# Optimization experiments

Hardware: AMD Instinct MI355X
Metric: run time of the kernel (lower is better)

Reference implementation:

```python
import jax, jax.numpy as jnp
from jax import lax
import numpy as np

STATE, ACT, TGT = 115, 39, 3
DIMS = [STATE + ACT, 16, 32, 64, 128, 64, 32, 16, 8, STATE]
B, T = 2048, 128


def setup_inputs() -> dict:
    key = jax.random.key(0)
    ks = jax.random.split(key, 2 * 9 + 3)
    inp = {"u": jax.random.normal(ks[0], (B, T, STATE + ACT), jnp.float32)}
    for i in range(9):
        fi, fo = DIMS[i], DIMS[i + 1]
        s = 1.0 / np.sqrt(fi)
        inp[f"W{i}"] = jax.random.uniform(ks[2 * i + 1], (fi, fo), jnp.float32, -s, s)
        inp[f"b{i}"] = jax.random.uniform(ks[2 * i + 2], (fo,), jnp.float32, -s, s)
    s = 1.0 / np.sqrt(STATE)
    inp["Wr"] = jax.random.uniform(ks[-2], (STATE, TGT), jnp.float32, -s, s)
    inp["br"] = jax.random.uniform(ks[-1], (TGT,), jnp.float32, -s, s)
    return inp


def reference(u, W0, b0, W1, b1, W2, b2, W3, b3, W4, b4, W5, b5, W6, b6, W7, b7, W8, b8, Wr, br):
    Ws = [W0, W1, W2, W3, W4, W5, W6, W7, W8]
    bs = [b0, b1, b2, b3, b4, b5, b6, b7, b8]

    def mlp(h):
        # 8 hidden Linear+ReLU6 layers, final Linear with no activation
        for i in range(8):
            h = jnp.clip(h @ Ws[i] + bs[i], 0.0, 6.0)  # ReLU6
        return h @ Ws[8] + bs[8]

    x0 = u[:, 0, :STATE]                      # [B, S]
    acts = jnp.swapaxes(u[:, :, -ACT:], 0, 1)  # [T, B, A]

    def step(x, a):
        xn = x + mlp(jnp.concatenate([x, a], axis=1))  # residual update
        return xn, xn

    _, xs = lax.scan(step, x0, acts)          # xs: [T, B, S] = x[:,1:,:]
    x_full = jnp.concatenate([x0[None], xs], axis=0)      # [T+1, B, S]
    x_full = jnp.swapaxes(x_full, 0, 1)                   # [B, T+1, S]

    r = x_full[:, 1:, :] @ Wr + br                        # [B, T, TGT]
    reward = -jnp.sqrt(jnp.sum(r * r, axis=2, keepdims=True))  # [B, T, 1]
    return jnp.concatenate([x_full[:, :-1, :], reward], axis=2)  # [B, T, S+1]
```

## Files before the change

### kernel.cpp

```cpp
#include <hip/hip_runtime.h>
#include <math.h>


#define TSTEPS 128
#define NB     2048
#define NST    115
#define NACT   39
#define NINF   154
#define NOUTF  116
constexpr int NT   = 256;
constexpr int ROWS = 4;

template<int CTRL>
__device__ __forceinline__ float dpp_add(float x) {
  int y = __builtin_amdgcn_update_dpp(0, __float_as_int(x), CTRL, 0xF, 0xF, true);
  return x + __int_as_float(y);
}
template<int KS>
__device__ __forceinline__ float kreduce(float a) {
  if constexpr (KS >= 2)  a = dpp_add<0xB1>(a);
  if constexpr (KS >= 4)  a = dpp_add<0x4E>(a);
  if constexpr (KS >= 8)  a = dpp_add<0x141>(a);
  if constexpr (KS >= 16) a = dpp_add<0x140>(a);
  return a;
}

__device__ __forceinline__ void barrier_lds() {
  asm volatile("s_waitcnt lgkmcnt(0)\n\ts_barrier" ::: "memory");
}
__device__ __forceinline__ void wait_lds() {
  asm volatile("s_waitcnt lgkmcnt(0)" ::: "memory");
}

template<int K, int NW, int NP, int NC, int KS, int RS, int J>
__device__ __forceinline__ void wload(const float* __restrict__ Wg,
                                      const float* __restrict__ bg,
                                      float (&w)[J][NC], float (&b)[NC], int tid) {
  static_assert(NP * KS * RS == NT, "bad cfg");
  constexpr float BS = 1.0f / (float)KS;
  const int kp = tid % KS, rest = tid / KS, cg = rest % NP;
#pragma unroll
  for (int j = 0; j < J; ++j)
#pragma unroll
    for (int c = 0; c < NC; ++c) {
      const int k = kp + KS * j, n = cg + c * NP;
      w[j][c] = (k < K && n < NW) ? Wg[k * NW + n] : 0.f;
    }
#pragma unroll
  for (int c = 0; c < NC; ++c) {
    const int n = cg + c * NP;
    b[c] = (n < NW) ? bg[n] * BS : 0.f;
  }
}

template<int K, int NW, int NP, int NC, int KS, int RS, int J, bool CLIP>
__device__ __forceinline__ void lrun(const float (&w)[J][NC], const float (&b)[NC],
                                     const float* __restrict__ in,
                                     float* __restrict__ out, int tid) {
  constexpr int RPL = ROWS / RS;
  const int kp = tid % KS, rest = tid / KS, cg = rest % NP, rg = rest / NP;
  float acc[NC][RPL];
#pragma unroll
  for (int c = 0; c < NC; ++c)
#pragma unroll
    for (int r = 0; r < RPL; ++r) acc[c][r] = b[c];

#pragma unroll
  for (int j = 0; j < J; ++j) {
    const int k = kp + KS * j;
    const float* ap = in + k * ROWS + rg * RPL;
    float av[RPL];
    if constexpr (RPL == 4) {
      float4 t = *(const float4*)ap; av[0]=t.x; av[1]=t.y; av[2]=t.z; av[3]=t.w;
    } else if constexpr (RPL == 2) {
      float2 t = *(const float2*)ap; av[0]=t.x; av[1]=t.y;
    } else {
      av[0] = *ap;
    }
#pragma unroll
    for (int c = 0; c < NC; ++c)
#pragma unroll
      for (int r = 0; r < RPL; ++r) acc[c][r] += w[j][c] * av[r];
  }
#pragma unroll
  for (int c = 0; c < NC; ++c)
#pragma unroll
    for (int r = 0; r < RPL; ++r) acc[c][r] = kreduce<KS>(acc[c][r]);

  if (kp == 0) {
#pragma unroll
    for (int c = 0; c < NC; ++c) {
      const int n = cg + c * NP;
      bool ok = true;
      if constexpr (NP * NC > NW) ok = (n < NW);
      if (ok) {
        float ov[RPL];
#pragma unroll
        for (int r = 0; r < RPL; ++r) {
          float v = acc[c][r];
          if constexpr (CLIP) v = __builtin_amdgcn_fmed3f(v, 0.f, 6.f);
          ov[r] = v;
        }
        float* op = out + n * ROWS + rg * RPL;
        if constexpr (RPL == 4)      *(float4*)op = make_float4(ov[0], ov[1], ov[2], ov[3]);
        else if constexpr (RPL == 2) *(float2*)op = make_float2(ov[0], ov[1]);
        else                         *op = ov[0];
      }
    }
  }
}

__global__ __launch_bounds__(NT, 2)
void worldnet_kernel(const float* __restrict__ u,
                     const float* __restrict__ W0, const float* __restrict__ b0,
                     const float* __restrict__ W1, const float* __restrict__ b1,
                     const float* __restrict__ W2, const float* __restrict__ b2,
                     const float* __restrict__ W3, const float* __restrict__ b3,
                     const float* __restrict__ W4, const float* __restrict__ b4,
                     const float* __restrict__ W5, const float* __restrict__ b5,
                     const float* __restrict__ W6, const float* __restrict__ b6,
                     const float* __restrict__ W7, const float* __restrict__ b7,
                     const float* __restrict__ W8, const float* __restrict__ b8,
                     const float* __restrict__ Wr, const float* __restrict__ br,
                     float* __restrict__ out) {
  __shared__ __align__(16) float sIN[160 * ROWS];
  __shared__ __align__(16) float sA[128 * ROWS];
  __shared__ __align__(16) float sB[128 * ROWS];
  const int tid = threadIdx.x, wv = tid >> 6, lane = tid & 63;

  float w0[10][1], w1[2][1], w2[4][2], w3[8][4], w4[8][4],
        w5[4][2],  w6[2][1], w7[1][1], w8[4][1], wR[8][1];
  float c0[1], c1[1], c2[2], c3[4], c4[4], c5[2], c6[1], c7[1], c8[1], cR[1];
  wload<154, 16,  16, 1, 16, 1, 10>(W0, b0, w0, c0, tid);
  wload< 16, 32,  32, 1,  8, 1,  2>(W1, b1, w1, c1, tid);
  wload< 32, 64,  32, 2,  8, 1,  4>(W2, b2, w2, c2, tid);
  wload< 64, 128, 32, 4,  8, 1,  8>(W3, b3, w3, c3, tid);
  wload<128, 64,  16, 4, 16, 1,  8>(W4, b4, w4, c4, tid);
  wload< 64, 32,  16, 2, 16, 1,  4>(W5, b5, w5, c5, tid);
  wload< 32, 16,  16, 1, 16, 1,  2>(W6, b6, w6, c6, tid);
  wload< 16,  8,   8, 1, 16, 2,  1>(W7, b7, w7, c7, tid);
  wload<  8, 115, 128, 1, 2, 1,  4>(W8, b8, w8, c8, tid);
  wload<115,  3,   4, 1, 16, 4,  8>(Wr, br, wR, cR, tid);

  const size_t row = (size_t)blockIdx.x * ROWS + wv;
  const float* urow = u + row * (size_t)(TSTEPS * NINF);
  float* orow = out + row * (size_t)(TSTEPS * NOUTF);

  sIN[lane * ROWS + wv] = urow[lane];
  orow[lane] = urow[lane];
  if (lane < NST - 64) {
    sIN[(lane + 64) * ROWS + wv] = urow[lane + 64];
    orow[lane + 64] = urow[lane + 64];
  }
  if (tid < (160 - NINF) * ROWS) sIN[NINF * ROWS + tid] = 0.f;
  float a_pre = (lane < NACT) ? urow[NST + lane] : 0.f;
  barrier_lds();

#pragma unroll 1
  for (int t = 0; t < TSTEPS; ++t) {
    float* ot = orow + (size_t)t * NOUTF;

    if (lane < NACT) sIN[(NST + lane) * ROWS + wv] = a_pre;
    {
      const int tn = (t < TSTEPS - 1) ? t + 1 : t;
      a_pre = (lane < NACT) ? urow[tn * NINF + NST + lane] : 0.f;
    }
    barrier_lds();

    lrun<154, 16,  16, 1, 16, 1, 10, true >(w0, c0, sIN, sA, tid); barrier_lds();
    lrun< 16, 32,  32, 1,  8, 1,  2, true >(w1, c1, sA, sB, tid); barrier_lds();
    lrun< 32, 64,  32, 2,  8, 1,  4, true >(w2, c2, sB, sA, tid); barrier_lds();
    lrun< 64, 128, 32, 4,  8, 1,  8, true >(w3, c3, sA, sB, tid); barrier_lds();
    lrun<128, 64,  16, 4, 16, 1,  8, true >(w4, c4, sB, sA, tid); barrier_lds();
    lrun< 64, 32,  16, 2, 16, 1,  4, true >(w5, c5, sA, sB, tid); barrier_lds();
    lrun< 32, 16,  16, 1, 16, 1,  2, true >(w6, c6, sB, sA, tid); barrier_lds();
    lrun< 16,  8,   8, 1, 16, 2,  1, true >(w7, c7, sA, sB, tid); barrier_lds();
    lrun<  8, 115, 128, 1, 2, 1,  4, false>(w8, c8, sB, sA, tid); barrier_lds();

    {
      const int i0 = lane * ROWS + wv, i1 = (lane + 64) * ROWS + wv;
      float xn0 = sIN[i0] + sA[i0];
      sIN[i0] = xn0;
      float xn1 = 0.f;
      if (lane < NST - 64) { xn1 = sIN[i1] + sA[i1]; sIN[i1] = xn1; }
      if (t < TSTEPS - 1) {
        float* on = ot + NOUTF;
        on[lane] = xn0;
        if (lane < NST - 64) on[lane + 64] = xn1;
      }
      wait_lds();

      const int kp = lane & 15;
      float p = cR[0];
#pragma unroll
      for (int j = 0; j < 8; ++j) {
        const int k = kp + 16 * j;
        p += wR[j][0] * sIN[k * ROWS + wv];
      }
      p = kreduce<16>(p);
      float s0 = __shfl(p, 0, 64);
      float s1 = __shfl(p, 16, 64);
      float s2 = __shfl(p, 32, 64);
      if (lane == 0) ot[NST] = -sqrtf(s0 * s0 + s1 * s1 + s2 * s2);
    }
  }
}

extern "C" void kernel_launch(void* const* d_in, const int* in_sizes, int n_in,
                              void* d_out, int out_size, void* d_ws, size_t ws_size,
                              hipStream_t stream) {
  const float* u  = (const float*)d_in[0];
  const float* W0 = (const float*)d_in[1];  const float* b0 = (const float*)d_in[2];
  const float* W1 = (const float*)d_in[3];  const float* b1 = (const float*)d_in[4];
  const float* W2 = (const float*)d_in[5];  const float* b2 = (const float*)d_in[6];
  const float* W3 = (const float*)d_in[7];  const float* b3 = (const float*)d_in[8];
  const float* W4 = (const float*)d_in[9];  const float* b4 = (const float*)d_in[10];
  const float* W5 = (const float*)d_in[11]; const float* b5 = (const float*)d_in[12];
  const float* W6 = (const float*)d_in[13]; const float* b6 = (const float*)d_in[14];
  const float* W7 = (const float*)d_in[15]; const float* b7 = (const float*)d_in[16];
  const float* W8 = (const float*)d_in[17]; const float* b8 = (const float*)d_in[18];
  const float* Wr = (const float*)d_in[19]; const float* br = (const float*)d_in[20];
  float* out = (float*)d_out;
  (void)in_sizes; (void)n_in; (void)out_size; (void)d_ws; (void)ws_size;

  dim3 grid(NB / ROWS), block(NT);
  hipLaunchKernelGGL(worldnet_kernel, grid, block, 0, stream,
                     u, W0, b0, W1, b1, W2, b2, W3, b3, W4, b4,
                     W5, b5, W6, b6, W7, b7, W8, b8, Wr, br, out);
}
```

Measured before the change: 772.1 us.

## Remap small layers to per-wave row partitioning and replace block barriers with LDS waits

Reworks the thread-to-work mapping of most MLP layers so that, for the narrow layers, each wave works only on its own batch row (RS=4). Those layers then need only an LDS wait instead of a full workgroup barrier. Full barriers are kept only around the wide middle layers, which still share work across waves. The residual state is also kept in registers (xr0/xr1), which removes LDS reads. The intent is to cut per-step barrier overhead, at the cost of more per-thread weight registers and less parallelism within each row for the narrow layers.

```diff
diff --git a/kernel.cpp b/kernel.cpp
--- a/kernel.cpp
+++ b/kernel.cpp
@@ -37,6 +37,7 @@
                                       const float* __restrict__ bg,
                                       float (&w)[J][NC], float (&b)[NC], int tid) {
   static_assert(NP * KS * RS == NT, "bad cfg");
+  static_assert(J * KS >= K, "bad J");
   constexpr float BS = 1.0f / (float)KS;
   const int kp = tid % KS, rest = tid / KS, cg = rest % NP;
 #pragma unroll
@@ -87,7 +88,7 @@
 #pragma unroll
     for (int r = 0; r < RPL; ++r) acc[c][r] = kreduce<KS>(acc[c][r]);
 
-  if (kp == 0) {
+  if (kp == 0 || KS == 1) {
 #pragma unroll
     for (int c = 0; c < NC; ++c) {
       const int n = cg + c * NP;
@@ -128,33 +129,35 @@
   __shared__ __align__(16) float sB[128 * ROWS];
   const int tid = threadIdx.x, wv = tid >> 6, lane = tid & 63;
 
-  float w0[10][1], w1[2][1], w2[4][2], w3[8][4], w4[8][4],
-        w5[4][2],  w6[2][1], w7[1][1], w8[4][1], wR[8][1];
-  float c0[1], c1[1], c2[2], c3[4], c4[4], c5[2], c6[1], c7[1], c8[1], cR[1];
-  wload<154, 16,  16, 1, 16, 1, 10>(W0, b0, w0, c0, tid);
-  wload< 16, 32,  32, 1,  8, 1,  2>(W1, b1, w1, c1, tid);
-  wload< 32, 64,  32, 2,  8, 1,  4>(W2, b2, w2, c2, tid);
-  wload< 64, 128, 32, 4,  8, 1,  8>(W3, b3, w3, c3, tid);
-  wload<128, 64,  16, 4, 16, 1,  8>(W4, b4, w4, c4, tid);
-  wload< 64, 32,  16, 2, 16, 1,  4>(W5, b5, w5, c5, tid);
-  wload< 32, 16,  16, 1, 16, 1,  2>(W6, b6, w6, c6, tid);
-  wload< 16,  8,   8, 1, 16, 2,  1>(W7, b7, w7, c7, tid);
-  wload<  8, 115, 128, 1, 2, 1,  4>(W8, b8, w8, c8, tid);
+  float w0[20][2], w1[8][1], w2[16][2], w3[16][2], w4[16][2],
+        w5[16][2], w6[8][1], w7[2][1],  w8[8][2],  wR[8][1];
+  float c0[2], c1[1], c2[2], c3[2], c4[2], c5[2], c6[1], c7[1], c8[2], cR[1];
+  wload<154, 16,   8, 2,  8, 4, 20>(W0, b0, w0, c0, tid);
+  wload< 16, 32,  32, 1,  2, 4,  8>(W1, b1, w1, c1, tid);
+  wload< 32, 64,  32, 2,  2, 4, 16>(W2, b2, w2, c2, tid);
+  wload< 64, 128, 64, 2,  4, 1, 16>(W3, b3, w3, c3, tid);
+  wload<128, 64,  32, 2,  8, 1, 16>(W4, b4, w4, c4, tid);
+  wload< 64, 32,  16, 2,  4, 4, 16>(W5, b5, w5, c5, tid);
+  wload< 32, 16,  16, 1,  4, 4,  8>(W6, b6, w6, c6, tid);
+  wload< 16,  8,   8, 1,  8, 4,  2>(W7, b7, w7, c7, tid);
+  wload<  8, 115, 64, 2,  1, 4,  8>(W8, b8, w8, c8, tid);
   wload<115,  3,   4, 1, 16, 4,  8>(Wr, br, wR, cR, tid);
 
   const size_t row = (size_t)blockIdx.x * ROWS + wv;
   const float* urow = u + row * (size_t)(TSTEPS * NINF);
   float* orow = out + row * (size_t)(TSTEPS * NOUTF);
 
-  sIN[lane * ROWS + wv] = urow[lane];
-  orow[lane] = urow[lane];
+  float xr0 = urow[lane];
+  float xr1 = (lane < NST - 64) ? urow[lane + 64] : 0.f;
+  sIN[lane * ROWS + wv] = xr0;
+  orow[lane] = xr0;
   if (lane < NST - 64) {
-    sIN[(lane + 64) * ROWS + wv] = urow[lane + 64];
-    orow[lane + 64] = urow[lane + 64];
-  }
-  if (tid < (160 - NINF) * ROWS) sIN[NINF * ROWS + tid] = 0.f;
+    sIN[(lane + 64) * ROWS + wv] = xr1;
+    orow[lane + 64] = xr1;
+  }
+  if (lane < 160 - NINF) sIN[(NINF + lane) * ROWS + wv] = 0.f;
   float a_pre = (lane < NACT) ? urow[NST + lane] : 0.f;
-  barrier_lds();
+  wait_lds();
 
 #pragma unroll 1
   for (int t = 0; t < TSTEPS; ++t) {
@@ -165,24 +168,31 @@
       const int tn = (t < TSTEPS - 1) ? t + 1 : t;
       a_pre = (lane < NACT) ? urow[tn * NINF + NST + lane] : 0.f;
     }
+    wait_lds();
+
+    lrun<154, 16,   8, 2,  8, 4, 20, true >(w0, c0, sIN, sA, tid); wait_lds();
+    lrun< 16, 32,  32, 1,  2, 4,  8, true >(w1, c1, sA, sB, tid); wait_lds();
+    lrun< 32, 64,  32, 2,  2, 4, 16, true >(w2, c2, sB, sA, tid);
     barrier_lds();
 
-    lrun<154, 16,  16, 1, 16, 1, 10, true >(w0, c0, sIN, sA, tid); barrier_lds();
-    lrun< 16, 32,  32, 1,  8, 1,  2, true >(w1, c1, sA, sB, tid); barrier_lds();
-    lrun< 32, 64,  32, 2,  8, 1,  4, true >(w2, c2, sB, sA, tid); barrier_lds();
-    lrun< 64, 128, 32, 4,  8, 1,  8, true >(w3, c3, sA, sB, tid); barrier_lds();
-    lrun<128, 64,  16, 4, 16, 1,  8, true >(w4, c4, sB, sA, tid); barrier_lds();
-    lrun< 64, 32,  16, 2, 16, 1,  4, true >(w5, c5, sA, sB, tid); barrier_lds();
-    lrun< 32, 16,  16, 1, 16, 1,  2, true >(w6, c6, sB, sA, tid); barrier_lds();
-    lrun< 16,  8,   8, 1, 16, 2,  1, true >(w7, c7, sA, sB, tid); barrier_lds();
-    lrun<  8, 115, 128, 1, 2, 1,  4, false>(w8, c8, sB, sA, tid); barrier_lds();
+    lrun< 64, 128, 64, 2,  4, 1, 16, true >(w3, c3, sA, sB, tid);
+    barrier_lds();
+    lrun<128, 64,  32, 2,  8, 1, 16, true >(w4, c4, sB, sA, tid);
+    barrier_lds();
+
+    lrun< 64, 32,  16, 2,  4, 4, 16, true >(w5, c5, sA, sB, tid); wait_lds();
+    lrun< 32, 16,  16, 1,  4, 4,  8, true >(w6, c6, sB, sA, tid); wait_lds();
+    lrun< 16,  8,   8, 1,  8, 4,  2, true >(w7, c7, sA, sB, tid); wait_lds();
+    lrun<  8, 115, 64, 2,  1, 4,  8, false>(w8, c8, sB, sA, tid); wait_lds();
 
     {
       const int i0 = lane * ROWS + wv, i1 = (lane + 64) * ROWS + wv;
-      float xn0 = sIN[i0] + sA[i0];
+      float xn0 = xr0 + sA[i0];
+      float xn1 = xr1 + sA[i1];
       sIN[i0] = xn0;
-      float xn1 = 0.f;
-      if (lane < NST - 64) { xn1 = sIN[i1] + sA[i1]; sIN[i1] = xn1; }
+      if (lane < NST - 64) sIN[i1] = xn1;
+      xr0 = xn0;
+      if (lane < NST - 64) xr1 = xn1;
       if (t < TSTEPS - 1) {
         float* on = ot + NOUTF;
         on[lane] = xn0;
```

Measured after the change: 957.6 us. 24.0% more time.

## Halve rows per block and keep residual state in registers

Applied to the files above, without the earlier changes.

Each block now handles two batch rows instead of four, and the launch-bounds occupancy target rises from 2 to 4, so twice as many blocks are in flight to hide the serial per-step LDS and barrier latency. Only the first two waves own rows: they keep the residual state in registers and skip re-reading it from LDS. The risk is register pressure, since the weight arrays must fit in the tighter per-thread budget, and spilling would hurt. Each wave also does less arithmetic per synchronisation.

```diff
diff --git a/kernel.cpp b/kernel.cpp
--- a/kernel.cpp
+++ b/kernel.cpp
@@ -9,7 +9,7 @@
 #define NINF   154
 #define NOUTF  116
 constexpr int NT   = 256;
-constexpr int ROWS = 4;
+constexpr int ROWS = 2;
 
 template<int CTRL>
 __device__ __forceinline__ float dpp_add(float x) {
@@ -37,6 +37,7 @@
                                       const float* __restrict__ bg,
                                       float (&w)[J][NC], float (&b)[NC], int tid) {
   static_assert(NP * KS * RS == NT, "bad cfg");
+  static_assert(J * KS >= K, "bad J");
   constexpr float BS = 1.0f / (float)KS;
   const int kp = tid % KS, rest = tid / KS, cg = rest % NP;
 #pragma unroll
@@ -70,9 +71,7 @@
     const int k = kp + KS * j;
     const float* ap = in + k * ROWS + rg * RPL;
     float av[RPL];
-    if constexpr (RPL == 4) {
-      float4 t = *(const float4*)ap; av[0]=t.x; av[1]=t.y; av[2]=t.z; av[3]=t.w;
-    } else if constexpr (RPL == 2) {
+    if constexpr (RPL == 2) {
       float2 t = *(const float2*)ap; av[0]=t.x; av[1]=t.y;
     } else {
       av[0] = *ap;
@@ -102,15 +101,14 @@
           ov[r] = v;
         }
         float* op = out + n * ROWS + rg * RPL;
-        if constexpr (RPL == 4)      *(float4*)op = make_float4(ov[0], ov[1], ov[2], ov[3]);
-        else if constexpr (RPL == 2) *(float2*)op = make_float2(ov[0], ov[1]);
-        else                         *op = ov[0];
+        if constexpr (RPL == 2) *(float2*)op = make_float2(ov[0], ov[1]);
+        else                    *op = ov[0];
       }
     }
   }
 }
 
-__global__ __launch_bounds__(NT, 2)
+__global__ __launch_bounds__(NT, 4)
 void worldnet_kernel(const float* __restrict__ u,
                      const float* __restrict__ W0, const float* __restrict__ b0,
                      const float* __restrict__ W1, const float* __restrict__ b1,
@@ -127,6 +125,8 @@
   __shared__ __align__(16) float sA[128 * ROWS];
   __shared__ __align__(16) float sB[128 * ROWS];
   const int tid = threadIdx.x, wv = tid >> 6, lane = tid & 63;
+  const int rwv = wv & 1;
+  const bool rowner = (wv < 2);
 
   float w0[10][1], w1[2][1], w2[4][2], w3[8][4], w4[8][4],
         w5[4][2],  w6[2][1], w7[1][1], w8[4][1], wR[8][1];
@@ -142,28 +142,33 @@
   wload<  8, 115, 128, 1, 2, 1,  4>(W8, b8, w8, c8, tid);
   wload<115,  3,   4, 1, 16, 4,  8>(Wr, br, wR, cR, tid);
 
-  const size_t row = (size_t)blockIdx.x * ROWS + wv;
+  const size_t row = (size_t)blockIdx.x * ROWS + rwv;
   const float* urow = u + row * (size_t)(TSTEPS * NINF);
   float* orow = out + row * (size_t)(TSTEPS * NOUTF);
 
-  sIN[lane * ROWS + wv] = urow[lane];
-  orow[lane] = urow[lane];
-  if (lane < NST - 64) {
-    sIN[(lane + 64) * ROWS + wv] = urow[lane + 64];
-    orow[lane + 64] = urow[lane + 64];
+  float xr0 = 0.f, xr1 = 0.f, a_pre = 0.f;
+  if (rowner) {
+    xr0 = urow[lane];
+    if (lane < NST - 64) xr1 = urow[lane + 64];
+    sIN[lane * ROWS + wv] = xr0;
+    orow[lane] = xr0;
+    if (lane < NST - 64) {
+      sIN[(lane + 64) * ROWS + wv] = xr1;
+      orow[lane + 64] = xr1;
+    }
+    if (lane < NACT) a_pre = urow[NST + lane];
   }
   if (tid < (160 - NINF) * ROWS) sIN[NINF * ROWS + tid] = 0.f;
-  float a_pre = (lane < NACT) ? urow[NST + lane] : 0.f;
-  barrier_lds();
+  wait_lds();
 
 #pragma unroll 1
   for (int t = 0; t < TSTEPS; ++t) {
     float* ot = orow + (size_t)t * NOUTF;
 
-    if (lane < NACT) sIN[(NST + lane) * ROWS + wv] = a_pre;
-    {
+    if (rowner) {
+      if (lane < NACT) sIN[(NST + lane) * ROWS + wv] = a_pre;
       const int tn = (t < TSTEPS - 1) ? t + 1 : t;
-      a_pre = (lane < NACT) ? urow[tn * NINF + NST + lane] : 0.f;
+      if (lane < NACT) a_pre = urow[tn * NINF + NST + lane];
     }
     barrier_lds();
 
@@ -177,12 +182,14 @@
     lrun< 16,  8,   8, 1, 16, 2,  1, true >(w7, c7, sA, sB, tid); barrier_lds();
     lrun<  8, 115, 128, 1, 2, 1,  4, false>(w8, c8, sB, sA, tid); barrier_lds();
 
-    {
+    if (rowner) {
       const int i0 = lane * ROWS + wv, i1 = (lane + 64) * ROWS + wv;
-      float xn0 = sIN[i0] + sA[i0];
+      float xn0 = xr0 + sA[i0];
+      float xn1 = xr1 + sA[i1];
       sIN[i0] = xn0;
-      float xn1 = 0.f;
-      if (lane < NST - 64) { xn1 = sIN[i1] + sA[i1]; sIN[i1] = xn1; }
+      if (lane < NST - 64) sIN[i1] = xn1;
+      xr0 = xn0;
+      if (lane < NST - 64) xr1 = xn1;
       if (t < TSTEPS - 1) {
         float* on = ot + NOUTF;
         on[lane] = xn0;
```

After: 1.973 ms. 155% more time.
